# Performance work log

Hardware: AMD Instinct MI355X
Metric: run time of the kernel (lower is better)

## Reference

```python
import jax, jax.numpy as jnp
import numpy as np

N = 25000      # number of target nodes
K = 32         # sampled neighbor fanout
F_IN = 256
F_OUT = 256


def setup_inputs() -> dict:
    key = jax.random.key(0)
    k1, k2, k3, k4 = jax.random.split(key, 4)
    x = jax.random.normal(k1, (N, F_IN), dtype=jnp.float32)
    neigh = jax.random.randint(k2, (N, K), 0, N, dtype=jnp.int64)
    # Linear(in_feats, out_feats) parameters
    W = jax.random.normal(k3, (F_IN, F_OUT), dtype=jnp.float32) / np.sqrt(F_IN)
    b = jax.random.normal(k4, (F_OUT,), dtype=jnp.float32) * 0.01
    return {"x": x, "neigh": neigh, "W": W, "b": b}


def reference(x, neigh, W, b):
    # Gather neighbor features: [N, K, F_IN]
    h = x[neigh]
    # Linear + ReLU transform on each neighbor feature
    h = jax.nn.relu(jnp.einsum('nkf,fo->nko', h, W) + b)
    # Element-wise max-pool across the neighbor set -> [N, F_OUT]
    return jnp.max(h, axis=1)
```

## Files before the change

kernel.cpp:

```cpp
#include <hip/hip_runtime.h>
#include <hip/hip_bf16.h>

#define N_NODES 25000
#define KFAN    32
#define FIN     256
#define FOUT    256

typedef float  f32x4  __attribute__((ext_vector_type(4)));
typedef short  s16x8  __attribute__((ext_vector_type(8)));
typedef short  s16x4  __attribute__((ext_vector_type(4)));

__device__ __forceinline__ ushort f2bf(float f) {
    unsigned int u = __float_as_uint(f);
    u += 0x7fffu + ((u >> 16) & 1u);
    return (ushort)(u >> 16);
}
__device__ __forceinline__ unsigned int pack2(float a, float b) {
    return (unsigned int)f2bf(a) | ((unsigned int)f2bf(b) << 16);
}

__global__ __launch_bounds__(256) void transpose_w(
    const float* __restrict__ W, ushort* __restrict__ Wt)
{
    __shared__ float ls[32][33];
    const int bid = blockIdx.x;
    const int kt  = bid & 7;
    const int nt  = bid >> 3;
    const int t   = threadIdx.x;

    {
        int kl = t >> 3, n4 = (t & 7) * 4;
        float4 v = *(const float4*)(W + (size_t)(kt * 32 + kl) * FOUT + nt * 32 + n4);
        ls[kl][n4 + 0] = v.x; ls[kl][n4 + 1] = v.y;
        ls[kl][n4 + 2] = v.z; ls[kl][n4 + 3] = v.w;
    }
    __syncthreads();
    {
        int nl = t >> 3, k4 = (t & 7) * 4;
        ushort4 o;
        o.x = f2bf(ls[k4 + 0][nl]);
        o.y = f2bf(ls[k4 + 1][nl]);
        o.z = f2bf(ls[k4 + 2][nl]);
        o.w = f2bf(ls[k4 + 3][nl]);
        *(ushort4*)(Wt + (size_t)(nt * 32 + nl) * FIN + kt * 32 + k4) = o;
    }
}

__global__ __launch_bounds__(256) void gemm_mfma(
    const float*  __restrict__ x,
    const ushort* __restrict__ Wt,
    const float*  __restrict__ bias,
    ushort*       __restrict__ y)
{
    __shared__ ushort As[32][72];

    const int tid  = threadIdx.x;
    const int lane = tid & 63;
    const int wv   = tid >> 6;
    const int l16  = lane & 15;
    const int q    = lane >> 4;
    const int row0 = blockIdx.x * 32;
    const int n0   = wv * 64;

    f32x4 acc[2][4];
    #pragma unroll
    for (int i = 0; i < 2; ++i)
        #pragma unroll
        for (int j = 0; j < 4; ++j) acc[i][j] = (f32x4)0.f;

    const int r    = tid >> 3;
    const int kcol = (tid & 7) * 8;

    for (int kc = 0; kc < FIN; kc += 64) {
        float4 v0 = make_float4(0.f, 0.f, 0.f, 0.f), v1 = v0;
        int gr = row0 + r;
        if (gr < N_NODES) {
            const float* p = x + (size_t)gr * FIN + kc + kcol;
            v0 = *(const float4*)p;
            v1 = *(const float4*)(p + 4);
        }
        uint4 pk;
        pk.x = pack2(v0.x, v0.y); pk.y = pack2(v0.z, v0.w);
        pk.z = pack2(v1.x, v1.y); pk.w = pack2(v1.z, v1.w);
        *(uint4*)&As[r][kcol] = pk;
        __syncthreads();

        #pragma unroll
        for (int kk = 0; kk < 64; kk += 32) {
            const int k0 = kk + q * 8;
            s16x8 a0 = *(const s16x8*)&As[l16][k0];
            s16x8 a1 = *(const s16x8*)&As[16 + l16][k0];
            #pragma unroll
            for (int ct = 0; ct < 4; ++ct) {
                const int n = n0 + ct * 16 + l16;
                s16x8 b = *(const s16x8*)(Wt + (size_t)n * FIN + kc + k0);
                acc[0][ct] = __builtin_amdgcn_mfma_f32_16x16x32_bf16(a0, b, acc[0][ct], 0, 0, 0);
                acc[1][ct] = __builtin_amdgcn_mfma_f32_16x16x32_bf16(a1, b, acc[1][ct], 0, 0, 0);
            }
        }
        __syncthreads();
    }

    #pragma unroll
    for (int ct = 0; ct < 4; ++ct) {
        const int col = n0 + ct * 16 + l16;
        const float bv = bias[col];
        #pragma unroll
        for (int mt = 0; mt < 2; ++mt) {
            #pragma unroll
            for (int rr = 0; rr < 4; ++rr) {
                int row = row0 + mt * 16 + q * 4 + rr;
                if (row < N_NODES)
                    y[(size_t)row * FOUT + col] = f2bf(fmaxf(acc[mt][ct][rr] + bv, 0.f));
            }
        }
    }
}

__global__ __launch_bounds__(256) void pool_max(
    const ushort* __restrict__ y,
    const int*    __restrict__ neigh,
    float*        __restrict__ out)
{
    const int bid   = blockIdx.x;
    const int chunk = bid & 3;
    const int nb    = bid >> 2;
    const int tid   = threadIdx.x;
    const int lane  = tid & 63;
    const int g     = lane >> 4;
    const int gl    = lane & 15;
    const int wv    = tid >> 6;

    const int n  = nb * 16 + wv * 4 + g;
    const int nc = n < N_NODES ? n : N_NODES - 1;

    const int* np = neigh + (size_t)nc * KFAN + gl * 2;
    const int i0 = np[0], i1 = np[1];
    const int base16 = lane & 48;

    const ushort* yc = y + chunk * 64 + gl * 4;

    s16x4 acc = {0, 0, 0, 0};
    #pragma unroll
    for (int k = 0; k < KFAN; ++k) {
        int src = base16 | (k >> 1);
        int idx = __shfl((k & 1) ? i1 : i0, src);
        s16x4 cur = *(const s16x4*)(yc + (size_t)idx * FOUT);
        acc = __builtin_elementwise_max(acc, cur);
    }

    if (n < N_NODES) {
        f32x4 o;
        o.x = __uint_as_float(((unsigned int)(ushort)acc.x) << 16);
        o.y = __uint_as_float(((unsigned int)(ushort)acc.y) << 16);
        o.z = __uint_as_float(((unsigned int)(ushort)acc.z) << 16);
        o.w = __uint_as_float(((unsigned int)(ushort)acc.w) << 16);
        __builtin_nontemporal_store(o, (f32x4*)(out + (size_t)n * FOUT + chunk * 64 + gl * 4));
    }
}

extern "C" void kernel_launch(void* const* d_in, const int* in_sizes, int n_in,
                              void* d_out, int out_size, void* d_ws, size_t ws_size,
                              hipStream_t stream) {
    const float* x     = (const float*)d_in[0];
    const int*   neigh = (const int*)  d_in[1];
    const float* W     = (const float*)d_in[2];
    const float* bias  = (const float*)d_in[3];
    float*       out   = (float*)d_out;
    ushort*      y     = (ushort*)d_ws;
    ushort*      Wt    = (ushort*)d_out;

    transpose_w<<<64, 256, 0, stream>>>(W, Wt);

    const int mblocks = (N_NODES + 31) / 32;
    gemm_mfma<<<mblocks, 256, 0, stream>>>(x, Wt, bias, y);

    const int nblocks = ((N_NODES + 15) / 16) * 4;
    pool_max<<<nblocks, 256, 0, stream>>>(y, neigh, out);
}
```

Measured before the change: 127.7 us.

## Retile GEMM to 64x128 blocks and widen pool gathers to 16-byte loads

The GEMM now uses a 2D grid where each block covers 64 rows and 128 output columns, and each wave computes a 64x32 tile. This changes the balance of A loads from LDS versus B loads from global, and x rows are now read twice, once per column half. The pooling kernel now has 8 lanes per node loading 8 bf16 values each (16 bytes) with int4 index loads, giving fewer, wider gather requests. The tradeoff is extra x traffic in the GEMM and different occupancy in exchange for better per-wave MFMA reuse and more efficient gathers.

```diff
diff --git a/kernel.cpp b/kernel.cpp
--- a/kernel.cpp
+++ b/kernel.cpp
@@ -8,7 +8,6 @@
 
 typedef float  f32x4  __attribute__((ext_vector_type(4)));
 typedef short  s16x8  __attribute__((ext_vector_type(8)));
-typedef short  s16x4  __attribute__((ext_vector_type(4)));
 
 __device__ __forceinline__ ushort f2bf(float f) {
     unsigned int u = __float_as_uint(f);
@@ -52,61 +51,69 @@
     const float*  __restrict__ bias,
     ushort*       __restrict__ y)
 {
-    __shared__ ushort As[32][72];
+    __shared__ ushort As[64][72];
 
     const int tid  = threadIdx.x;
     const int lane = tid & 63;
     const int wv   = tid >> 6;
     const int l16  = lane & 15;
     const int q    = lane >> 4;
-    const int row0 = blockIdx.x * 32;
-    const int n0   = wv * 64;
+    const int row0 = blockIdx.x * 64;
+    const int n0   = blockIdx.y * 128 + wv * 32;
 
-    f32x4 acc[2][4];
+    f32x4 acc[4][2];
     #pragma unroll
-    for (int i = 0; i < 2; ++i)
+    for (int i = 0; i < 4; ++i)
         #pragma unroll
-        for (int j = 0; j < 4; ++j) acc[i][j] = (f32x4)0.f;
+        for (int j = 0; j < 2; ++j) acc[i][j] = (f32x4)0.f;
 
-    const int r    = tid >> 3;
-    const int kcol = (tid & 7) * 8;
+    const int r    = tid >> 2;
+    const int kcol = (tid & 3) * 16;
 
     for (int kc = 0; kc < FIN; kc += 64) {
-        float4 v0 = make_float4(0.f, 0.f, 0.f, 0.f), v1 = v0;
+        float4 v0 = make_float4(0.f,0.f,0.f,0.f), v1 = v0, v2 = v0, v3 = v0;
         int gr = row0 + r;
         if (gr < N_NODES) {
             const float* p = x + (size_t)gr * FIN + kc + kcol;
             v0 = *(const float4*)p;
             v1 = *(const float4*)(p + 4);
+            v2 = *(const float4*)(p + 8);
+            v3 = *(const float4*)(p + 12);
         }
-        uint4 pk;
-        pk.x = pack2(v0.x, v0.y); pk.y = pack2(v0.z, v0.w);
-        pk.z = pack2(v1.x, v1.y); pk.w = pack2(v1.z, v1.w);
-        *(uint4*)&As[r][kcol] = pk;
+        uint4 pa, pb;
+        pa.x = pack2(v0.x, v0.y); pa.y = pack2(v0.z, v0.w);
+        pa.z = pack2(v1.x, v1.y); pa.w = pack2(v1.z, v1.w);
+        pb.x = pack2(v2.x, v2.y); pb.y = pack2(v2.z, v2.w);
+        pb.z = pack2(v3.x, v3.y); pb.w = pack2(v3.z, v3.w);
+        *(uint4*)&As[r][kcol]     = pa;
+        *(uint4*)&As[r][kcol + 8] = pb;
         __syncthreads();
 
         #pragma unroll
         for (int kk = 0; kk < 64; kk += 32) {
             const int k0 = kk + q * 8;
-            s16x8 a0 = *(const s16x8*)&As[l16][k0];
-            s16x8 a1 = *(const s16x8*)&As[16 + l16][k0];
+            s16x8 a[4], b[2];
             #pragma unroll
-            for (int ct = 0; ct < 4; ++ct) {
-                const int n = n0 + ct * 16 + l16;
-                s16x8 b = *(const s16x8*)(Wt + (size_t)n * FIN + kc + k0);
-                acc[0][ct] = __builtin_amdgcn_mfma_f32_16x16x32_bf16(a0, b, acc[0][ct], 0, 0, 0);
-                acc[1][ct] = __builtin_amdgcn_mfma_f32_16x16x32_bf16(a1, b, acc[1][ct], 0, 0, 0);
-            }
+            for (int mt = 0; mt < 4; ++mt)
+                a[mt] = *(const s16x8*)&As[mt * 16 + l16][k0];
+            #pragma unroll
+            for (int ct = 0; ct < 2; ++ct)
+                b[ct] = *(const s16x8*)(Wt + (size_t)(n0 + ct * 16 + l16) * FIN + kc + k0);
+            #pragma unroll
+            for (int mt = 0; mt < 4; ++mt)
+                #pragma unroll
+                for (int ct = 0; ct < 2; ++ct)
+                    acc[mt][ct] = __builtin_amdgcn_mfma_f32_16x16x32_bf16(a[mt], b[ct], acc[mt][ct], 0, 0, 0);
         }
         __syncthreads();
     }
 
     #pragma unroll
-    for (int ct = 0; ct < 4; ++ct) {
+    for (int ct = 0; ct < 2; ++ct) {
         const int col = n0 + ct * 16 + l16;
         const float bv = bias[col];
         #pragma unroll
-        for (int mt = 0; mt < 2; ++mt) {
+        for (int mt = 0; mt < 4; ++mt) {
             #pragma unroll
             for (int rr = 0; rr < 4; ++rr) {
                 int row = row0 + mt * 16 + q * 4 + rr;
@@ -127,35 +134,40 @@
     const int nb    = bid >> 2;
     const int tid   = threadIdx.x;
     const int lane  = tid & 63;
-    const int g     = lane >> 4;
-    const int gl    = lane & 15;
+    const int g     = lane >> 3;
+    const int gl    = lane & 7;
     const int wv    = tid >> 6;
 
-    const int n  = nb * 16 + wv * 4 + g;
+    const int n  = nb * 32 + wv * 8 + g;
     const int nc = n < N_NODES ? n : N_NODES - 1;
 
-    const int* np = neigh + (size_t)nc * KFAN + gl * 2;
-    const int i0 = np[0], i1 = np[1];
-    const int base16 = lane & 48;
+    const int4 iv = *(const int4*)(neigh + (size_t)nc * KFAN + gl * 4);
+    const int base8 = lane & 56;
+    int ia[4] = {iv.x, iv.y, iv.z, iv.w};
 
-    const ushort* yc = y + chunk * 64 + gl * 4;
+    const ushort* yc = y + chunk * 64 + gl * 8;
 
-    s16x4 acc = {0, 0, 0, 0};
+    s16x8 acc = (s16x8)0;
     #pragma unroll
     for (int k = 0; k < KFAN; ++k) {
-        int src = base16 | (k >> 1);
-        int idx = __shfl((k & 1) ? i1 : i0, src);
-        s16x4 cur = *(const s16x4*)(yc + (size_t)idx * FOUT);
+        int idx = __shfl(ia[k & 3], base8 + (k >> 2));
+        s16x8 cur = *(const s16x8*)(yc + (size_t)idx * FOUT);
         acc = __builtin_elementwise_max(acc, cur);
     }
 
     if (n < N_NODES) {
-        f32x4 o;
-        o.x = __uint_as_float(((unsigned int)(ushort)acc.x) << 16);
-        o.y = __uint_as_float(((unsigned int)(ushort)acc.y) << 16);
-        o.z = __uint_as_float(((unsigned int)(ushort)acc.z) << 16);
-        o.w = __uint_as_float(((unsigned int)(ushort)acc.w) << 16);
-        __builtin_nontemporal_store(o, (f32x4*)(out + (size_t)n * FOUT + chunk * 64 + gl * 4));
+        f32x4 o0, o1;
+        o0.x = __uint_as_float(((unsigned int)(ushort)acc[0]) << 16);
+        o0.y = __uint_as_float(((unsigned int)(ushort)acc[1]) << 16);
+        o0.z = __uint_as_float(((unsigned int)(ushort)acc[2]) << 16);
+        o0.w = __uint_as_float(((unsigned int)(ushort)acc[3]) << 16);
+        o1.x = __uint_as_float(((unsigned int)(ushort)acc[4]) << 16);
+        o1.y = __uint_as_float(((unsigned int)(ushort)acc[5]) << 16);
+        o1.z = __uint_as_float(((unsigned int)(ushort)acc[6]) << 16);
+        o1.w = __uint_as_float(((unsigned int)(ushort)acc[7]) << 16);
+        float* op = out + (size_t)n * FOUT + chunk * 64 + gl * 8;
+        __builtin_nontemporal_store(o0, (f32x4*)op);
+        __builtin_nontemporal_store(o1, (f32x4*)(op + 4));
     }
 }
 
@@ -172,9 +184,9 @@
 
     transpose_w<<<64, 256, 0, stream>>>(W, Wt);
 
-    const int mblocks = (N_NODES + 31) / 32;
-    gemm_mfma<<<mblocks, 256, 0, stream>>>(x, Wt, bias, y);
+    dim3 g1((N_NODES + 63) / 64, 2);
+    gemm_mfma<<<g1, 256, 0, stream>>>(x, Wt, bias, y);
 
-    const int nblocks = ((N_NODES + 15) / 16) * 4;
+    const int nblocks = ((N_NODES + 31) / 32) * 4;
     pool_max<<<nblocks, 256, 0, stream>>>(y, neigh, out);
 }
```

Result: faster. 117.7 us (-7.8%).
